# Kernel tuning notes

Measured on AMD Instinct MI355X. Metric: run time of the kernel, lower is better.

The kernel has to match this reference:

```python
import jax, jax.numpy as jnp
import numpy as np

NUM_HEADS = 16
SCALE = 0.125  # head_dim ** -0.5, head_dim = 64


def setup_inputs() -> dict:
    key = jax.random.key(0)
    kq, kk, kv = jax.random.split(key, 3)
    B, N, C = 32, 2048, 64  # B = batch(2) * num_heads(16)
    return {
        "query": jax.random.normal(kq, (B, N, C), dtype=jnp.float32),
        "key": jax.random.normal(kk, (B, N, C), dtype=jnp.float32),
        "value": jax.random.normal(kv, (B, N, C), dtype=jnp.float32),
    }


def reference(query, key, value):
    B, N, C = query.shape
    # baddbmm with beta=0, alpha=scale -> scale * (q @ k^T): [B, N, N]
    scores = SCALE * jnp.einsum("bnc,bmc->bnm", query, key)
    probs = jax.nn.softmax(scores, axis=2).astype(value.dtype)
    hidden = jnp.einsum("bnm,bmc->bnc", probs, value)  # [B, N, C]
    # [B, N, C] -> [B//H, H, N, C] -> [B//H, N, H, C] -> [B//H, N, H*C]
    h = hidden.reshape(B // NUM_HEADS, NUM_HEADS, N, C)
    h = jnp.transpose(h, (0, 2, 1, 3)).reshape(B // NUM_HEADS, N, C * NUM_HEADS)
    return h
```

## Files before the change

kernel.cpp:

```cpp
#include <hip/hip_runtime.h>


using f16 = _Float16;
typedef __attribute__((ext_vector_type(4))) f16   f16x4;
typedef __attribute__((ext_vector_type(8))) f16   f16x8;
typedef __attribute__((ext_vector_type(4))) float f32x4;

constexpr int   N    = 2048;
constexpr float SL2E = 0.125f * 1.4426950408889634f;
constexpr int   KSTR = 72;
constexpr int   VSTR = 68;

__global__ __launch_bounds__(256, 4) void fattn(const float* __restrict__ Qg,
                                                const float* __restrict__ Kg,
                                                const float* __restrict__ Vg,
                                                float* __restrict__ Og)
{
    __shared__ alignas(16) char smem[(2 * 64 * KSTR + 2 * 64 * VSTR) * 2];

    const int tid  = threadIdx.x;
    const int wave = tid >> 6;
    const int lane = tid & 63;
    const int g    = lane >> 4;
    const int qi   = lane & 15;

    const int swz = (blockIdx.x & 7) * 128 + (blockIdx.x >> 3);
    const int bh = swz >> 5;
    const int qt = swz & 31;

    const size_t base = (size_t)bh * N * 64;
    const float4* K4 = reinterpret_cast<const float4*>(Kg + base);
    const float4* V4 = reinterpret_cast<const float4*>(Vg + base);

    const int    qrow = qt * 64 + wave * 16 + qi;
    const float* Qrow = Qg + base + (size_t)qrow * 64;
    f16x8 qf[2];
#pragma unroll
    for (int kb = 0; kb < 2; ++kb) {
        float4 x0 = *reinterpret_cast<const float4*>(Qrow + kb * 32 + 8 * g);
        float4 x1 = *reinterpret_cast<const float4*>(Qrow + kb * 32 + 8 * g + 4);
        qf[kb] = f16x8{(f16)(x0.x * SL2E), (f16)(x0.y * SL2E), (f16)(x0.z * SL2E), (f16)(x0.w * SL2E),
                       (f16)(x1.x * SL2E), (f16)(x1.y * SL2E), (f16)(x1.z * SL2E), (f16)(x1.w * SL2E)};
    }

    float m_run = -INFINITY;
    float l_run = 0.f;
    f32x4 acc[4] = {};

    float4 kr[4], vr[4];
    auto LOAD = [&](int kv0) {
#pragma unroll
        for (int i = 0; i < 4; ++i) {
            int idx = tid + 256 * i, row = idx >> 4, c4 = idx & 15;
            kr[i] = K4[(size_t)(kv0 + row) * 16 + c4];
            vr[i] = V4[(size_t)(kv0 + row) * 16 + c4];
        }
    };
    auto STORE = [&](int b) {
        f16 (*kl)[KSTR] = reinterpret_cast<f16(*)[KSTR]>(smem + b * 64 * KSTR * 2);
        f16 (*vt)[VSTR] = reinterpret_cast<f16(*)[VSTR]>(smem + (2 * 64 * KSTR + b * 64 * VSTR) * 2);
#pragma unroll
        for (int i = 0; i < 4; ++i) {
            int idx = tid + 256 * i, row = idx >> 4, c4 = idx & 15;
            float4 a = kr[i];
            *reinterpret_cast<f16x4*>(&kl[row][c4 * 4]) =
                f16x4{(f16)a.x, (f16)a.y, (f16)a.z, (f16)a.w};
            float4 v = vr[i];
            vt[c4 * 4 + 0][row] = (f16)v.x;
            vt[c4 * 4 + 1][row] = (f16)v.y;
            vt[c4 * 4 + 2][row] = (f16)v.z;
            vt[c4 * 4 + 3][row] = (f16)v.w;
        }
    };

    LOAD(0);
    STORE(0);
    __syncthreads();

    for (int t = 0; t < 32; ++t) {
        const int cur = t & 1;
        if (t < 31) LOAD((t + 1) * 64);

        f16 (*kl)[KSTR] = reinterpret_cast<f16(*)[KSTR]>(smem + cur * 64 * KSTR * 2);
        f16 (*vt)[VSTR] = reinterpret_cast<f16(*)[VSTR]>(smem + (2 * 64 * KSTR + cur * 64 * VSTR) * 2);

        f32x4 st[4];
        __builtin_amdgcn_s_setprio(1);
#pragma unroll
        for (int t2 = 0; t2 < 4; ++t2) {
            f32x4 a = {0.f, 0.f, 0.f, 0.f};
#pragma unroll
            for (int kb = 0; kb < 2; ++kb) {
                f16x8 kf = *reinterpret_cast<const f16x8*>(&kl[t2 * 16 + qi][kb * 32 + 8 * g]);
                a = __builtin_amdgcn_mfma_f32_16x16x32_f16(kf, qf[kb], a, 0, 0, 0);
            }
            st[t2] = a;
        }
        __builtin_amdgcn_s_setprio(0);

        float mt = -INFINITY;
#pragma unroll
        for (int t2 = 0; t2 < 4; ++t2)
#pragma unroll
            for (int r = 0; r < 4; ++r) mt = fmaxf(mt, st[t2][r]);
        mt = fmaxf(mt, __shfl_xor(mt, 16));
        mt = fmaxf(mt, __shfl_xor(mt, 32));
        const float mnew = fmaxf(m_run, mt);
        const float corr = __builtin_amdgcn_exp2f(m_run - mnew);

        float ps = 0.f;
        f16x4 pf[4];
#pragma unroll
        for (int t2 = 0; t2 < 4; ++t2)
#pragma unroll
            for (int r = 0; r < 4; ++r) {
                float p = __builtin_amdgcn_exp2f(st[t2][r] - mnew);
                ps += p;
                pf[t2][r] = (f16)p;
            }
        ps += __shfl_xor(ps, 16);
        ps += __shfl_xor(ps, 32);
        l_run = l_run * corr + ps;
        m_run = mnew;
#pragma unroll
        for (int dt = 0; dt < 4; ++dt)
#pragma unroll
            for (int r = 0; r < 4; ++r) acc[dt][r] *= corr;

        __builtin_amdgcn_s_setprio(1);
#pragma unroll
        for (int dt = 0; dt < 4; ++dt)
#pragma unroll
            for (int t2 = 0; t2 < 4; ++t2) {
                f16x4 vf = *reinterpret_cast<const f16x4*>(&vt[dt * 16 + qi][t2 * 16 + 4 * g]);
                acc[dt] = __builtin_amdgcn_mfma_f32_16x16x16f16(vf, pf[t2], acc[dt], 0, 0, 0);
            }
        __builtin_amdgcn_s_setprio(0);

        if (t < 31) {
            STORE(cur ^ 1);
            __syncthreads();
        }
    }

    const float inv_l = 1.f / l_run;
    __syncthreads();
    float (*ot)[68] = reinterpret_cast<float(*)[68]>(smem + (size_t)wave * 16 * 68 * sizeof(float));
#pragma unroll
    for (int dt = 0; dt < 4; ++dt)
#pragma unroll
        for (int r = 0; r < 4; ++r)
            ot[qi][dt * 16 + 4 * g + r] = acc[dt][r] * inv_l;

    const int b = bh >> 4, h = bh & 15;
#pragma unroll
    for (int i = 0; i < 4; ++i) {
        int row = i * 4 + g;
        int n   = qt * 64 + wave * 16 + row;
        float4 val = *reinterpret_cast<const float4*>(&ot[row][4 * qi]);
        float4* dst = reinterpret_cast<float4*>(Og + ((size_t)b * N + n) * 1024 + h * 64) + qi;
        *dst = val;
    }
}

extern "C" void kernel_launch(void* const* d_in, const int* in_sizes, int n_in,
                              void* d_out, int out_size, void* d_ws, size_t ws_size,
                              hipStream_t stream) {
    const float* Q = (const float*)d_in[0];
    const float* K = (const float*)d_in[1];
    const float* V = (const float*)d_in[2];
    float* O = (float*)d_out;
    fattn<<<dim3(32 * 32), dim3(256), 0, stream>>>(Q, K, V, O);
}
```

Before: 164.8 us.

## Use XOR-swizzled LDS layouts, packed f16 conversion, and skip unneeded rescales

Drops the padded K and transposed-V shared-memory layouts in favour of unpadded XOR-swizzled layouts. V is now loaded so each thread holds four rows of one column and can write f16x4 vectors instead of scalar transposed stores, which cuts LDS store instructions and bank conflicts. Conversions to f16 use packed cvt_pkrtz, which rounds toward zero. The online-softmax rescale of acc and l is skipped when no lane's max increased, which adds a wave-uniform branch.

```diff
diff --git a/kernel.cpp b/kernel.cpp
--- a/kernel.cpp
+++ b/kernel.cpp
@@ -2,21 +2,25 @@
 
 
 using f16 = _Float16;
+typedef __attribute__((ext_vector_type(2))) f16   f16x2;
 typedef __attribute__((ext_vector_type(4))) f16   f16x4;
 typedef __attribute__((ext_vector_type(8))) f16   f16x8;
 typedef __attribute__((ext_vector_type(4))) float f32x4;
 
+static __device__ __forceinline__ f16x2 pk(float a, float b) {
+    return __builtin_bit_cast(f16x2, __builtin_amdgcn_cvt_pkrtz(a, b));
+}
+
 constexpr int   N    = 2048;
 constexpr float SL2E = 0.125f * 1.4426950408889634f;
-constexpr int   KSTR = 72;
-constexpr int   VSTR = 68;
+
 
 __global__ __launch_bounds__(256, 4) void fattn(const float* __restrict__ Qg,
                                                 const float* __restrict__ Kg,
                                                 const float* __restrict__ Vg,
                                                 float* __restrict__ Og)
 {
-    __shared__ alignas(16) char smem[(2 * 64 * KSTR + 2 * 64 * VSTR) * 2];
+    __shared__ alignas(16) char smem[32768];
 
     const int tid  = threadIdx.x;
     const int wave = tid >> 6;
@@ -29,47 +33,63 @@
     const int qt = swz & 31;
 
     const size_t base = (size_t)bh * N * 64;
-    const float4* K4 = reinterpret_cast<const float4*>(Kg + base);
-    const float4* V4 = reinterpret_cast<const float4*>(Vg + base);
+    const f32x4* K4 = reinterpret_cast<const f32x4*>(Kg + base);
+    const f32x4* V4 = reinterpret_cast<const f32x4*>(Vg + base);
 
     const int    qrow = qt * 64 + wave * 16 + qi;
     const float* Qrow = Qg + base + (size_t)qrow * 64;
     f16x8 qf[2];
 #pragma unroll
     for (int kb = 0; kb < 2; ++kb) {
-        float4 x0 = *reinterpret_cast<const float4*>(Qrow + kb * 32 + 8 * g);
-        float4 x1 = *reinterpret_cast<const float4*>(Qrow + kb * 32 + 8 * g + 4);
-        qf[kb] = f16x8{(f16)(x0.x * SL2E), (f16)(x0.y * SL2E), (f16)(x0.z * SL2E), (f16)(x0.w * SL2E),
-                       (f16)(x1.x * SL2E), (f16)(x1.y * SL2E), (f16)(x1.z * SL2E), (f16)(x1.w * SL2E)};
+        f32x4 x0 = *reinterpret_cast<const f32x4*>(Qrow + kb * 32 + 8 * g);
+        f32x4 x1 = *reinterpret_cast<const f32x4*>(Qrow + kb * 32 + 8 * g + 4);
+        qf[kb] = f16x8{(f16)(x0[0] * SL2E), (f16)(x0[1] * SL2E), (f16)(x0[2] * SL2E), (f16)(x0[3] * SL2E),
+                       (f16)(x1[0] * SL2E), (f16)(x1[1] * SL2E), (f16)(x1[2] * SL2E), (f16)(x1[3] * SL2E)};
+    }
+
+    const int voff  = 64 * (tid >> 4) + (tid & 15);
+    const int vrow4 = tid >> 4;
+    const int vc4   = tid & 15;
+
+    int vswz[4], vrow[4];
+#pragma unroll
+    for (int dt = 0; dt < 4; ++dt) {
+        int d = dt * 16 + qi;
+        vswz[dt] = (d ^ (d >> 2)) & 15;
+        vrow[dt] = d * 128;
     }
 
     float m_run = -INFINITY;
     float l_run = 0.f;
     f32x4 acc[4] = {};
 
-    float4 kr[4], vr[4];
+    f32x4 kr[4], vr[4];
     auto LOAD = [&](int kv0) {
+#pragma unroll
+        for (int i = 0; i < 4; ++i) kr[i] = K4[kv0 * 16 + tid + 256 * i];
+#pragma unroll
+        for (int j = 0; j < 4; ++j) vr[j] = V4[kv0 * 16 + voff + 16 * j];
+    };
+    auto STORE = [&](int b) {
+        char* kb_ = smem + b * 8192;
+        char* vb_ = smem + 16384 + b * 8192;
 #pragma unroll
         for (int i = 0; i < 4; ++i) {
             int idx = tid + 256 * i, row = idx >> 4, c4 = idx & 15;
-            kr[i] = K4[(size_t)(kv0 + row) * 16 + c4];
-            vr[i] = V4[(size_t)(kv0 + row) * 16 + c4];
-        }
-    };
-    auto STORE = [&](int b) {
-        f16 (*kl)[KSTR] = reinterpret_cast<f16(*)[KSTR]>(smem + b * 64 * KSTR * 2);
-        f16 (*vt)[VSTR] = reinterpret_cast<f16(*)[VSTR]>(smem + (2 * 64 * KSTR + b * 64 * VSTR) * 2);
-#pragma unroll
-        for (int i = 0; i < 4; ++i) {
-            int idx = tid + 256 * i, row = idx >> 4, c4 = idx & 15;
-            float4 a = kr[i];
-            *reinterpret_cast<f16x4*>(&kl[row][c4 * 4]) =
-                f16x4{(f16)a.x, (f16)a.y, (f16)a.z, (f16)a.w};
-            float4 v = vr[i];
-            vt[c4 * 4 + 0][row] = (f16)v.x;
-            vt[c4 * 4 + 1][row] = (f16)v.y;
-            vt[c4 * 4 + 2][row] = (f16)v.z;
-            vt[c4 * 4 + 3][row] = (f16)v.w;
+            f16x2 lo = pk(kr[i][0], kr[i][1]);
+            f16x2 hi = pk(kr[i][2], kr[i][3]);
+            f16x4 w  = __builtin_shufflevector(lo, hi, 0, 1, 2, 3);
+            int off = row * 128 + (((c4 >> 1) ^ (row & 7)) << 4) + ((c4 & 1) << 3);
+            *reinterpret_cast<f16x4*>(kb_ + off) = w;
+        }
+#pragma unroll
+        for (int jj = 0; jj < 4; ++jj) {
+            int d = vc4 * 4 + jj;
+            f16x2 lo = pk(vr[0][jj], vr[1][jj]);
+            f16x2 hi = pk(vr[2][jj], vr[3][jj]);
+            f16x4 w  = __builtin_shufflevector(lo, hi, 0, 1, 2, 3);
+            int off = d * 128 + ((vrow4 ^ ((d ^ (d >> 2)) & 15)) << 3);
+            *reinterpret_cast<f16x4*>(vb_ + off) = w;
         }
     };
 
@@ -81,18 +101,20 @@
         const int cur = t & 1;
         if (t < 31) LOAD((t + 1) * 64);
 
-        f16 (*kl)[KSTR] = reinterpret_cast<f16(*)[KSTR]>(smem + cur * 64 * KSTR * 2);
-        f16 (*vt)[VSTR] = reinterpret_cast<f16(*)[VSTR]>(smem + (2 * 64 * KSTR + cur * 64 * VSTR) * 2);
+        const char* kb_ = smem + cur * 8192;
+        const char* vb_ = smem + 16384 + cur * 8192;
 
         f32x4 st[4];
         __builtin_amdgcn_s_setprio(1);
 #pragma unroll
         for (int t2 = 0; t2 < 4; ++t2) {
             f32x4 a = {0.f, 0.f, 0.f, 0.f};
+            int row = t2 * 16 + qi;
 #pragma unroll
             for (int kb = 0; kb < 2; ++kb) {
-                f16x8 kf = *reinterpret_cast<const f16x8*>(&kl[t2 * 16 + qi][kb * 32 + 8 * g]);
-                a = __builtin_amdgcn_mfma_f32_16x16x32_f16(kf, qf[kb], a, 0, 0, 0);
+                int c16 = (4 * kb + g) ^ (row & 7);
+                f16x8 kk = *reinterpret_cast<const f16x8*>(kb_ + row * 128 + c16 * 16);
+                a = __builtin_amdgcn_mfma_f32_16x16x32_f16(kk, qf[kb], a, 0, 0, 0);
             }
             st[t2] = a;
         }
@@ -105,34 +127,42 @@
             for (int r = 0; r < 4; ++r) mt = fmaxf(mt, st[t2][r]);
         mt = fmaxf(mt, __shfl_xor(mt, 16));
         mt = fmaxf(mt, __shfl_xor(mt, 32));
-        const float mnew = fmaxf(m_run, mt);
-        const float corr = __builtin_amdgcn_exp2f(m_run - mnew);
+
+        if (!__all(mt <= m_run)) {
+            const float mnew = fmaxf(m_run, mt);
+            const float corr = __builtin_amdgcn_exp2f(m_run - mnew);
+            l_run *= corr;
+#pragma unroll
+            for (int dt = 0; dt < 4; ++dt)
+#pragma unroll
+                for (int r = 0; r < 4; ++r) acc[dt][r] *= corr;
+            m_run = mnew;
+        }
 
         float ps = 0.f;
         f16x4 pf[4];
 #pragma unroll
-        for (int t2 = 0; t2 < 4; ++t2)
-#pragma unroll
-            for (int r = 0; r < 4; ++r) {
-                float p = __builtin_amdgcn_exp2f(st[t2][r] - mnew);
-                ps += p;
-                pf[t2][r] = (f16)p;
-            }
+        for (int t2 = 0; t2 < 4; ++t2) {
+            float p0 = __builtin_amdgcn_exp2f(st[t2][0] - m_run);
+            float p1 = __builtin_amdgcn_exp2f(st[t2][1] - m_run);
+            float p2 = __builtin_amdgcn_exp2f(st[t2][2] - m_run);
+            float p3 = __builtin_amdgcn_exp2f(st[t2][3] - m_run);
+            ps += (p0 + p1) + (p2 + p3);
+            f16x2 lo = pk(p0, p1);
+            f16x2 hi = pk(p2, p3);
+            pf[t2] = __builtin_shufflevector(lo, hi, 0, 1, 2, 3);
+        }
         ps += __shfl_xor(ps, 16);
         ps += __shfl_xor(ps, 32);
-        l_run = l_run * corr + ps;
-        m_run = mnew;
+        l_run += ps;
+
+        __builtin_amdgcn_s_setprio(1);
 #pragma unroll
         for (int dt = 0; dt < 4; ++dt)
 #pragma unroll
-            for (int r = 0; r < 4; ++r) acc[dt][r] *= corr;
-
-        __builtin_amdgcn_s_setprio(1);
-#pragma unroll
-        for (int dt = 0; dt < 4; ++dt)
-#pragma unroll
             for (int t2 = 0; t2 < 4; ++t2) {
-                f16x4 vf = *reinterpret_cast<const f16x4*>(&vt[dt * 16 + qi][t2 * 16 + 4 * g]);
+                int c = (t2 * 4 + g) ^ vswz[dt];
+                f16x4 vf = *reinterpret_cast<const f16x4*>(vb_ + vrow[dt] + c * 8);
                 acc[dt] = __builtin_amdgcn_mfma_f32_16x16x16f16(vf, pf[t2], acc[dt], 0, 0, 0);
             }
         __builtin_amdgcn_s_setprio(0);
@@ -157,8 +187,8 @@
     for (int i = 0; i < 4; ++i) {
         int row = i * 4 + g;
         int n   = qt * 64 + wave * 16 + row;
-        float4 val = *reinterpret_cast<const float4*>(&ot[row][4 * qi]);
-        float4* dst = reinterpret_cast<float4*>(Og + ((size_t)b * N + n) * 1024 + h * 64) + qi;
+        f32x4 val = *reinterpret_cast<const f32x4*>(&ot[row][4 * qi]);
+        f32x4* dst = reinterpret_cast<f32x4*>(Og + ((size_t)b * N + n) * 1024 + h * 64) + qi;
         *dst = val;
     }
 }
```

Result: faster. 159.5 us (-3.2%).
